# Performance work log

Measured on AMD Instinct MI355X. Metric: run time of the kernel, lower is better.

Reference implementation:

```python
import jax, jax.numpy as jnp
import numpy as np

N = 50000        # n_nodes
E = 1_600_000    # n_edges (avg degree 32)
IN = 128         # in_dim
H = 8            # num_heads
R = 16           # hidden_rank
D = 16           # out_dim (per head)
SCALE = float(np.sqrt(D))


def setup_inputs() -> dict:
    key = jax.random.key(0)
    k1, k2, k3, k4, k5, k6 = jax.random.split(key, 6)
    h = jax.random.normal(k1, (N, IN), jnp.float32)
    src = jax.random.randint(k2, (E,), 0, N, dtype=jnp.int32)
    dst = jax.random.randint(k3, (E,), 0, N, dtype=jnp.int32)
    s = 1.0 / np.sqrt(IN)  # kaiming-ish scale
    p = jax.random.normal(k4, (IN, H * R), jnp.float32) * s
    q = jax.random.normal(k5, (IN, H * R), jnp.float32) * s
    Wv = jax.random.normal(k6, (IN, H * D), jnp.float32) * s
    return {"h": h, "src": src, "dst": dst, "p": p, "q": q, "Wv": Wv}


def reference(h, src, dst, p, q, Wv):
    # global_attention_type == 'transform' -> atted = h
    K = (h @ q).reshape(N, H, R)   # K_h = atted @ _q
    Q = (h @ p).reshape(N, H, R)   # Q_h = h @ _p
    V = (h @ Wv).reshape(N, H, D)  # V_h = V(h), no bias
    # per-edge score: (K[src] * Q[dst]).sum(-1, keepdim), then scaled exp
    score = jnp.sum(K[src] * Q[dst], axis=-1, keepdims=True)   # [E, H, 1]
    score = jnp.exp(jnp.clip(score / SCALE, -5.0, 5.0))
    # scatter-sum into destination nodes
    wV = jax.ops.segment_sum(V[src] * score, dst, num_segments=N)  # [N, H, D]
    z = jax.ops.segment_sum(score, dst, num_segments=N)            # [N, H, 1]
    z = jnp.where(z == 0, jnp.float32(0.001), z)
    return wV / z
```

## Files before the change

### kernel.cpp

```cpp
#include <hip/hip_runtime.h>
#include <hip/hip_fp16.h>


#define HNODE 64
#define EPB   8192
#define BKT_SHIFT 7
#define BKT_CAP 5120

typedef _Float16 f16x8 __attribute__((ext_vector_type(8)));
typedef float    f32x4 __attribute__((ext_vector_type(4)));
typedef _Float16 hv2   __attribute__((ext_vector_type(2)));

__device__ __forceinline__ float fdot2(unsigned a, unsigned b, float c) {
#if __has_builtin(__builtin_amdgcn_fdot2)
    return __builtin_amdgcn_fdot2(__builtin_bit_cast(hv2, a),
                                  __builtin_bit_cast(hv2, b), c, false);
#else
    __half2 ah = *(__half2*)&a, bh = *(__half2*)&b;
    float2 af = __half22float2(ah), bf = __half22float2(bh);
    return c + af.x * bf.x + af.y * bf.y;
#endif
}

__device__ __forceinline__ float2 h2f(unsigned u) {
    __half2 hh = *(__half2*)&u;
    return __half22float2(hh);
}

__device__ __forceinline__ unsigned pack2(float a, float b) {
    __half2 hh = __floats2half2_rn(a, b);
    return *(unsigned*)&hh;
}

__global__ __launch_bounds__(256) void wt_convert_kernel(
    const float* __restrict__ Wq, const float* __restrict__ Wp,
    const float* __restrict__ Wv, __half* __restrict__ Wt)
{
    int o = blockIdx.x * 256 + threadIdx.x;
    int m = o >> 14, rem = o & 16383;
    int nn = rem >> 7, kk = rem & 127;
    const float* W = (m == 0) ? Wq : (m == 1) ? Wp : Wv;
    Wt[o] = __float2half(W[kk * 128 + nn]);
}

__global__ __launch_bounds__(256) void gemm_kqv_kernel(
    const float* __restrict__ h, const __half* __restrict__ Wt,
    unsigned* __restrict__ KV, __half* __restrict__ Q, int n)
{
    __shared__ __align__(16) _Float16 ws[128 * 136];

    const int t = threadIdx.x;
    const int wid = t >> 6, lane = t & 63;
    const int node0 = blockIdx.x * HNODE;
    const int mrow = lane & 15, quad = lane >> 4;

    const int row = node0 + wid * 16 + mrow;
    const bool rowvalid = (row < n);
    const int rowc = rowvalid ? row : (n - 1);

    f16x8 hfr[4];
    #pragma unroll
    for (int s = 0; s < 4; s++) {
        const float4* hp = (const float4*)(h + (size_t)rowc * 128 + quad * 8 + 32 * s);
        float4 f0 = hp[0], f1 = hp[1];
        f16x8 a;
        a[0] = (_Float16)f0.x; a[1] = (_Float16)f0.y;
        a[2] = (_Float16)f0.z; a[3] = (_Float16)f0.w;
        a[4] = (_Float16)f1.x; a[5] = (_Float16)f1.y;
        a[6] = (_Float16)f1.z; a[7] = (_Float16)f1.w;
        hfr[s] = a;
    }

    f32x4 acc[3][8];
    #pragma unroll
    for (int m = 0; m < 3; m++)
        #pragma unroll
        for (int ct = 0; ct < 8; ct++) acc[m][ct] = (f32x4){0.f, 0.f, 0.f, 0.f};

    #pragma unroll
    for (int m = 0; m < 3; m++) {
        __syncthreads();
        {
            const uint4* wg = (const uint4*)(Wt + (size_t)m * 16384);
            #pragma unroll
            for (int i = 0; i < 8; i++) {
                int idx = t * 8 + i;
                int r = idx >> 4, seg = idx & 15;
                *(uint4*)(ws + r * 136 + seg * 8) = wg[idx];
            }
        }
        __syncthreads();
        #pragma unroll
        for (int s = 0; s < 4; s++) {
            #pragma unroll
            for (int ct = 0; ct < 8; ct++) {
                f16x8 a = *(const f16x8*)(ws + (ct * 16 + mrow) * 136 + quad * 8 + 32 * s);
                acc[m][ct] = __builtin_amdgcn_mfma_f32_16x16x32_f16(a, hfr[s], acc[m][ct], 0, 0, 0);
            }
        }
    }

    if (rowvalid) {
        unsigned* kvrow = KV + (size_t)row * 128;
        __half*   qrow  = Q  + (size_t)row * 128;
        #pragma unroll
        for (int ct = 0; ct < 8; ct++) {
            int qd = ct * 4 + quad;
            uint4 ov;
            ov.x = pack2(acc[0][ct][0], acc[0][ct][1]);
            ov.y = pack2(acc[0][ct][2], acc[0][ct][3]);
            ov.z = pack2(acc[2][ct][0], acc[2][ct][1]);
            ov.w = pack2(acc[2][ct][2], acc[2][ct][3]);
            *(uint4*)(kvrow + 4 * qd) = ov;
            uint2 qv;
            qv.x = pack2(acc[1][ct][0], acc[1][ct][1]);
            qv.y = pack2(acc[1][ct][2], acc[1][ct][3]);
            *(uint2*)(qrow + 4 * qd) = qv;
        }
    }
}

__global__ __launch_bounds__(256) void bucket_scatter_kernel(
    const int* __restrict__ src, const int* __restrict__ dst,
    int* __restrict__ bucket_cursor, int2* __restrict__ ebuf, int E, int nbkt)
{
    __shared__ int cnt[512];
    __shared__ int start[512];
    int t = threadIdx.x;
    for (int i = t; i < nbkt; i += 256) cnt[i] = 0;
    __syncthreads();

    int4 sv[8], dv[8];
    int base = blockIdx.x * EPB + t * 4;
    #pragma unroll
    for (int r = 0; r < 8; r++) {
        int i = base + r * 1024;
        if (i + 3 < E) {
            sv[r] = *(const int4*)(src + i);
            dv[r] = *(const int4*)(dst + i);
        } else {
            int ts[4], td[4];
            for (int k = 0; k < 4; k++) {
                int j = i + k;
                ts[k] = (j < E) ? src[j] : 0;
                td[k] = (j < E) ? dst[j] : -1;
            }
            sv[r] = make_int4(ts[0], ts[1], ts[2], ts[3]);
            dv[r] = make_int4(td[0], td[1], td[2], td[3]);
        }
        if (dv[r].x >= 0) atomicAdd(&cnt[dv[r].x >> BKT_SHIFT], 1);
        if (dv[r].y >= 0) atomicAdd(&cnt[dv[r].y >> BKT_SHIFT], 1);
        if (dv[r].z >= 0) atomicAdd(&cnt[dv[r].z >> BKT_SHIFT], 1);
        if (dv[r].w >= 0) atomicAdd(&cnt[dv[r].w >> BKT_SHIFT], 1);
    }
    __syncthreads();
    for (int i = t; i < nbkt; i += 256) {
        int c = cnt[i];
        start[i] = c ? atomicAdd(&bucket_cursor[i], c) : 0;
        cnt[i] = 0;
    }
    __syncthreads();
    #pragma unroll
    for (int r = 0; r < 8; r++) {
        int s, d, b, pl;
        d = dv[r].x; if (d >= 0) { s = sv[r].x; b = d >> BKT_SHIFT; pl = start[b] + atomicAdd(&cnt[b], 1); if (pl < BKT_CAP) ebuf[(size_t)b * BKT_CAP + pl] = make_int2(s, d); }
        d = dv[r].y; if (d >= 0) { s = sv[r].y; b = d >> BKT_SHIFT; pl = start[b] + atomicAdd(&cnt[b], 1); if (pl < BKT_CAP) ebuf[(size_t)b * BKT_CAP + pl] = make_int2(s, d); }
        d = dv[r].z; if (d >= 0) { s = sv[r].z; b = d >> BKT_SHIFT; pl = start[b] + atomicAdd(&cnt[b], 1); if (pl < BKT_CAP) ebuf[(size_t)b * BKT_CAP + pl] = make_int2(s, d); }
        d = dv[r].w; if (d >= 0) { s = sv[r].w; b = d >> BKT_SHIFT; pl = start[b] + atomicAdd(&cnt[b], 1); if (pl < BKT_CAP) ebuf[(size_t)b * BKT_CAP + pl] = make_int2(s, d); }
    }
}

__global__ __launch_bounds__(256) void fine_scatter_kernel(
    const int2* __restrict__ ebuf, const int* __restrict__ bucket_cursor,
    int2* __restrict__ offs, int* __restrict__ csr, int N, int nbkt)
{
    __shared__ int ldeg[128];
    __shared__ int lcur[128];
    int b = blockIdx.x, t = threadIdx.x;
    int node_base = b << BKT_SHIFT;
    int seg0 = b * BKT_CAP;
    int cnt = bucket_cursor[b];
    if (cnt > BKT_CAP) cnt = BKT_CAP;

    if (t < 128) ldeg[t] = 0;
    __syncthreads();
    for (int i = t; i < cnt; i += 256)
        atomicAdd(&ldeg[ebuf[seg0 + i].y - node_base], 1);
    __syncthreads();
    int mydeg = (t < 128) ? ldeg[t] : 0;
    for (int off = 1; off < 128; off <<= 1) {
        int y = (t >= off && t < 128) ? ldeg[t - off] : 0;
        __syncthreads();
        if (t < 128) ldeg[t] += y;
        __syncthreads();
    }
    if (t < 128) {
        int incl = ldeg[t];
        int gbeg = seg0 + incl - mydeg;
        lcur[t] = gbeg;
        int node = node_base + t;
        if (node < N) offs[node] = make_int2(gbeg, seg0 + incl);
    }
    __syncthreads();
    for (int i = t; i < cnt; i += 256) {
        int2 ed = ebuf[seg0 + i];
        int pos = atomicAdd(&lcur[ed.y - node_base], 1);
        csr[pos] = ed.x;
    }
}

__global__ __launch_bounds__(256) void aggregate_kernel(
    const uint4* __restrict__ KV, const uint2* __restrict__ Qr,
    const int2* __restrict__ offs, const int* __restrict__ csr,
    float4* __restrict__ out, int n)
{
    int t = threadIdx.x;
    int node = blockIdx.x * 4 + (t >> 6);
    if (node >= n) return;
    int lane = t & 63;
    int l = lane & 31;
    int eh = lane >> 5;

    uint2 qq = Qr[(size_t)node * 32 + l];
    int2 be = offs[node];
    int beg = be.x, cnt = be.y - be.x;

    float4 accV = make_float4(0.f, 0.f, 0.f, 0.f);
    float accZ = 0.f;

    int chunkbase = 0;
    int myidx = (beg + lane < be.y) ? csr[beg + lane] : 0;

    uint4 kv = make_uint4(0, 0, 0, 0);
    if (cnt > 0) {
        int s0 = __shfl(myidx, eh, 64);
        kv = KV[(size_t)s0 * 32 + l];
    }

    for (int e = 0; e < cnt; e += 2) {
        uint4 nkv;
        bool more = (e + 2 < cnt);
        if (more) {
            int off = e + 2 - chunkbase;
            if (off == 64) {
                chunkbase = e + 2;
                myidx = (beg + chunkbase + lane < be.y) ? csr[beg + chunkbase + lane] : 0;
                off = 0;
            }
            int sn = __shfl(myidx, off + eh, 64);
            nkv = KV[(size_t)sn * 32 + l];
        }
        float p = fdot2(kv.x, qq.x, fdot2(kv.y, qq.y, 0.f));
        p += __shfl_xor(p, 1);
        p += __shfl_xor(p, 2);
        float x = fminf(fmaxf(p * 0.25f, -5.f), 5.f);
        float sc = (e + eh < cnt) ? __expf(x) : 0.f;
        accZ += sc;
        float2 va = h2f(kv.z), vb = h2f(kv.w);
        accV.x += sc * va.x; accV.y += sc * va.y;
        accV.z += sc * vb.x; accV.w += sc * vb.y;
        if (more) kv = nkv;
    }

    accZ  += __shfl_xor(accZ, 32);
    accV.x += __shfl_xor(accV.x, 32);
    accV.y += __shfl_xor(accV.y, 32);
    accV.z += __shfl_xor(accV.z, 32);
    accV.w += __shfl_xor(accV.w, 32);

    if (lane < 32) {
        if (accZ == 0.f) accZ = 0.001f;
        float inv = 1.0f / accZ;
        out[(size_t)node * 32 + l] =
            make_float4(accV.x * inv, accV.y * inv, accV.z * inv, accV.w * inv);
    }
}


extern "C" void kernel_launch(void* const* d_in, const int* in_sizes, int n_in,
                              void* d_out, int out_size, void* d_ws, size_t ws_size,
                              hipStream_t stream)
{
    const float* h   = (const float*)d_in[0];
    const int*   src = (const int*)d_in[1];
    const int*   dst = (const int*)d_in[2];
    const float* p   = (const float*)d_in[3];
    const float* q   = (const float*)d_in[4];
    const float* wv  = (const float*)d_in[5];
    float* out = (float*)d_out;

    const int N = in_sizes[0] / 128;
    const int E = in_sizes[1];
    const int nbkt = (N + 127) >> BKT_SHIFT;

    unsigned* KV = (unsigned*)d_ws;
    __half* Qh   = (__half*)(KV + (size_t)N * 128);
    int2* ebuf   = (int2*)(Qh + (size_t)N * 128);
    int* csr     = (int*)(ebuf + (size_t)nbkt * BKT_CAP);
    int2* offs   = (int2*)(csr + (size_t)nbkt * BKT_CAP);
    int* bucket_cursor = (int*)(offs + N);
    __half* Wt   = (__half*)(bucket_cursor + 512);

    (void)hipMemsetAsync(bucket_cursor, 0, 512 * sizeof(int), stream);

    wt_convert_kernel<<<192, 256, 0, stream>>>(q, p, wv, Wt);

    int nblk_e = (E + EPB - 1) / EPB;
    bucket_scatter_kernel<<<nblk_e, 256, 0, stream>>>(src, dst, bucket_cursor, ebuf, E, nbkt);

    gemm_kqv_kernel<<<(N + HNODE - 1) / HNODE, 256, 0, stream>>>(h, Wt, KV, Qh, N);

    fine_scatter_kernel<<<nbkt, 256, 0, stream>>>(ebuf, bucket_cursor, offs, csr, N, nbkt);

    aggregate_kernel<<<(N + 3) / 4, 256, 0, stream>>>(
        (const uint4*)KV, (const uint2*)Qh, offs, csr, (float4*)out, N);
}
```

Baseline: 252.8 us.

## Pack edge buffer to 32-bit, reuse atomic ranks, deepen aggregate prefetch

Bucket scatter now keeps the rank returned by the first shared-memory atomic, so the second atomic pass is gone. Each edge is stored as one packed 32-bit word (7-bit local dst, 18-bit src) instead of an int2, which halves ebuf traffic. Fine scatter holds the edges in registers (up to 20 per thread) and reuses its atomic ranks, so ebuf is read once and the second atomic pass is dropped. The aggregate kernel prefetches two edge-pairs ahead instead of one to hide gather latency. This costs more registers, and the packing assumes N < 2^18 and at most 5120 edges per bucket.

```diff
diff --git a/kernel.cpp b/kernel.cpp
--- a/kernel.cpp
+++ b/kernel.cpp
@@ -122,7 +122,7 @@
 
 __global__ __launch_bounds__(256) void bucket_scatter_kernel(
     const int* __restrict__ src, const int* __restrict__ dst,
-    int* __restrict__ bucket_cursor, int2* __restrict__ ebuf, int E, int nbkt)
+    int* __restrict__ bucket_cursor, unsigned* __restrict__ ebuf, int E, int nbkt)
 {
     __shared__ int cnt[512];
     __shared__ int start[512];
@@ -130,7 +130,7 @@
     for (int i = t; i < nbkt; i += 256) cnt[i] = 0;
     __syncthreads();
 
-    int4 sv[8], dv[8];
+    int4 sv[8], dv[8], rk[8];
     int base = blockIdx.x * EPB + t * 4;
     #pragma unroll
     for (int r = 0; r < 8; r++) {
@@ -148,34 +148,33 @@
             sv[r] = make_int4(ts[0], ts[1], ts[2], ts[3]);
             dv[r] = make_int4(td[0], td[1], td[2], td[3]);
         }
-        if (dv[r].x >= 0) atomicAdd(&cnt[dv[r].x >> BKT_SHIFT], 1);
-        if (dv[r].y >= 0) atomicAdd(&cnt[dv[r].y >> BKT_SHIFT], 1);
-        if (dv[r].z >= 0) atomicAdd(&cnt[dv[r].z >> BKT_SHIFT], 1);
-        if (dv[r].w >= 0) atomicAdd(&cnt[dv[r].w >> BKT_SHIFT], 1);
+        rk[r].x = (dv[r].x >= 0) ? atomicAdd(&cnt[dv[r].x >> BKT_SHIFT], 1) : 0;
+        rk[r].y = (dv[r].y >= 0) ? atomicAdd(&cnt[dv[r].y >> BKT_SHIFT], 1) : 0;
+        rk[r].z = (dv[r].z >= 0) ? atomicAdd(&cnt[dv[r].z >> BKT_SHIFT], 1) : 0;
+        rk[r].w = (dv[r].w >= 0) ? atomicAdd(&cnt[dv[r].w >> BKT_SHIFT], 1) : 0;
     }
     __syncthreads();
     for (int i = t; i < nbkt; i += 256) {
         int c = cnt[i];
         start[i] = c ? atomicAdd(&bucket_cursor[i], c) : 0;
-        cnt[i] = 0;
     }
     __syncthreads();
     #pragma unroll
     for (int r = 0; r < 8; r++) {
-        int s, d, b, pl;
-        d = dv[r].x; if (d >= 0) { s = sv[r].x; b = d >> BKT_SHIFT; pl = start[b] + atomicAdd(&cnt[b], 1); if (pl < BKT_CAP) ebuf[(size_t)b * BKT_CAP + pl] = make_int2(s, d); }
-        d = dv[r].y; if (d >= 0) { s = sv[r].y; b = d >> BKT_SHIFT; pl = start[b] + atomicAdd(&cnt[b], 1); if (pl < BKT_CAP) ebuf[(size_t)b * BKT_CAP + pl] = make_int2(s, d); }
-        d = dv[r].z; if (d >= 0) { s = sv[r].z; b = d >> BKT_SHIFT; pl = start[b] + atomicAdd(&cnt[b], 1); if (pl < BKT_CAP) ebuf[(size_t)b * BKT_CAP + pl] = make_int2(s, d); }
-        d = dv[r].w; if (d >= 0) { s = sv[r].w; b = d >> BKT_SHIFT; pl = start[b] + atomicAdd(&cnt[b], 1); if (pl < BKT_CAP) ebuf[(size_t)b * BKT_CAP + pl] = make_int2(s, d); }
+        int s, d, b, pos;
+        d = dv[r].x; if (d >= 0) { s = sv[r].x; b = d >> BKT_SHIFT; pos = start[b] + rk[r].x; if (pos < BKT_CAP) ebuf[(size_t)b * BKT_CAP + pos] = ((unsigned)(d & 127) << 18) | (unsigned)s; }
+        d = dv[r].y; if (d >= 0) { s = sv[r].y; b = d >> BKT_SHIFT; pos = start[b] + rk[r].y; if (pos < BKT_CAP) ebuf[(size_t)b * BKT_CAP + pos] = ((unsigned)(d & 127) << 18) | (unsigned)s; }
+        d = dv[r].z; if (d >= 0) { s = sv[r].z; b = d >> BKT_SHIFT; pos = start[b] + rk[r].z; if (pos < BKT_CAP) ebuf[(size_t)b * BKT_CAP + pos] = ((unsigned)(d & 127) << 18) | (unsigned)s; }
+        d = dv[r].w; if (d >= 0) { s = sv[r].w; b = d >> BKT_SHIFT; pos = start[b] + rk[r].w; if (pos < BKT_CAP) ebuf[(size_t)b * BKT_CAP + pos] = ((unsigned)(d & 127) << 18) | (unsigned)s; }
     }
 }
 
 __global__ __launch_bounds__(256) void fine_scatter_kernel(
-    const int2* __restrict__ ebuf, const int* __restrict__ bucket_cursor,
+    const unsigned* __restrict__ ebuf, const int* __restrict__ bucket_cursor,
     int2* __restrict__ offs, int* __restrict__ csr, int N, int nbkt)
 {
     __shared__ int ldeg[128];
-    __shared__ int lcur[128];
+    __shared__ int lstart[128];
     int b = blockIdx.x, t = threadIdx.x;
     int node_base = b << BKT_SHIFT;
     int seg0 = b * BKT_CAP;
@@ -184,9 +183,19 @@
 
     if (t < 128) ldeg[t] = 0;
     __syncthreads();
-    for (int i = t; i < cnt; i += 256)
-        atomicAdd(&ldeg[ebuf[seg0 + i].y - node_base], 1);
-    __syncthreads();
+
+    unsigned pv[20];
+    int rk[20];
+    #pragma unroll
+    for (int j = 0; j < 20; j++) {
+        int i = t + j * 256;
+        bool ok = (i < cnt);
+        unsigned v = ok ? ebuf[seg0 + i] : 0u;
+        pv[j] = v;
+        rk[j] = ok ? atomicAdd(&ldeg[v >> 18], 1) : 0;
+    }
+    __syncthreads();
+
     int mydeg = (t < 128) ? ldeg[t] : 0;
     for (int off = 1; off < 128; off <<= 1) {
         int y = (t >= off && t < 128) ? ldeg[t - off] : 0;
@@ -195,17 +204,18 @@
         __syncthreads();
     }
     if (t < 128) {
-        int incl = ldeg[t];
-        int gbeg = seg0 + incl - mydeg;
-        lcur[t] = gbeg;
+        int gbeg = seg0 + ldeg[t] - mydeg;
+        lstart[t] = gbeg;
         int node = node_base + t;
-        if (node < N) offs[node] = make_int2(gbeg, seg0 + incl);
-    }
-    __syncthreads();
-    for (int i = t; i < cnt; i += 256) {
-        int2 ed = ebuf[seg0 + i];
-        int pos = atomicAdd(&lcur[ed.y - node_base], 1);
-        csr[pos] = ed.x;
+        if (node < N) offs[node] = make_int2(gbeg, gbeg + mydeg);
+    }
+    __syncthreads();
+
+    #pragma unroll
+    for (int j = 0; j < 20; j++) {
+        int i = t + j * 256;
+        if (i < cnt)
+            csr[lstart[pv[j] >> 18] + rk[j]] = (int)(pv[j] & 0x3FFFFu);
     }
 }
 
@@ -231,38 +241,36 @@
     int chunkbase = 0;
     int myidx = (beg + lane < be.y) ? csr[beg + lane] : 0;
 
-    uint4 kv = make_uint4(0, 0, 0, 0);
-    if (cnt > 0) {
-        int s0 = __shfl(myidx, eh, 64);
-        kv = KV[(size_t)s0 * 32 + l];
-    }
+    uint4 kvA = make_uint4(0, 0, 0, 0), kvB = make_uint4(0, 0, 0, 0);
+    if (cnt > 0) kvA = KV[(size_t)__shfl(myidx, eh, 64) * 32 + l];
+    if (cnt > 2) kvB = KV[(size_t)__shfl(myidx, 2 + eh, 64) * 32 + l];
 
     for (int e = 0; e < cnt; e += 2) {
         uint4 nkv;
-        bool more = (e + 2 < cnt);
+        bool more = (e + 4 < cnt);
         if (more) {
-            int off = e + 2 - chunkbase;
+            int off = e + 4 - chunkbase;
             if (off == 64) {
-                chunkbase = e + 2;
+                chunkbase += 64;
                 myidx = (beg + chunkbase + lane < be.y) ? csr[beg + chunkbase + lane] : 0;
                 off = 0;
             }
-            int sn = __shfl(myidx, off + eh, 64);
-            nkv = KV[(size_t)sn * 32 + l];
-        }
-        float p = fdot2(kv.x, qq.x, fdot2(kv.y, qq.y, 0.f));
+            nkv = KV[(size_t)__shfl(myidx, off + eh, 64) * 32 + l];
+        }
+        float p = fdot2(kvA.x, qq.x, fdot2(kvA.y, qq.y, 0.f));
         p += __shfl_xor(p, 1);
         p += __shfl_xor(p, 2);
         float x = fminf(fmaxf(p * 0.25f, -5.f), 5.f);
         float sc = (e + eh < cnt) ? __expf(x) : 0.f;
         accZ += sc;
-        float2 va = h2f(kv.z), vb = h2f(kv.w);
+        float2 va = h2f(kvA.z), vb = h2f(kvA.w);
         accV.x += sc * va.x; accV.y += sc * va.y;
         accV.z += sc * vb.x; accV.w += sc * vb.y;
-        if (more) kv = nkv;
-    }
-
-    accZ  += __shfl_xor(accZ, 32);
+        kvA = kvB;
+        if (more) kvB = nkv;
+    }
+
+    accZ   += __shfl_xor(accZ, 32);
     accV.x += __shfl_xor(accV.x, 32);
     accV.y += __shfl_xor(accV.y, 32);
     accV.z += __shfl_xor(accV.z, 32);
@@ -295,7 +303,7 @@
 
     unsigned* KV = (unsigned*)d_ws;
     __half* Qh   = (__half*)(KV + (size_t)N * 128);
-    int2* ebuf   = (int2*)(Qh + (size_t)N * 128);
+    unsigned* ebuf = (unsigned*)(Qh + (size_t)N * 128);
     int* csr     = (int*)(ebuf + (size_t)nbkt * BKT_CAP);
     int2* offs   = (int2*)(csr + (size_t)nbkt * BKT_CAP);
     int* bucket_cursor = (int*)(offs + N);
```

Measured after the change: 253.0 us. Within noise of the previous version (+0.1%).
